# Kernel tuning notes

Hardware: AMD Instinct MI355X
Metric: run time of the kernel (lower is better)

The kernel has to match this reference:

```python
import jax, jax.numpy as jnp
import numpy as np
from jax import lax

B, S, N, F = 64, 512, 30, 1
H, HD = 2, 8              # n_heads, head_dim (gat_hidden=16)
GH = H * HD               # gat_hidden
P = 64                    # projection_dim
LH = 64                   # lstm_hidden
ALPHA = 0.2


def setup_inputs() -> dict:
    key = jax.random.key(0)
    ks = jax.random.split(key, 16)
    x = jax.random.normal(ks[0], (B, S, N, F), dtype=jnp.float32)
    adj = jax.random.randint(ks[1], (N, N), 0, 2).astype(jnp.float32)
    adj = jnp.maximum(adj, jnp.eye(N, dtype=jnp.float32))  # self-loops, no empty rows
    sc = 0.1
    W_gat = sc * jax.random.normal(ks[2], (H, F, HD), dtype=jnp.float32)
    a_src = sc * jax.random.normal(ks[3], (H, HD), dtype=jnp.float32)
    a_dst = sc * jax.random.normal(ks[4], (H, HD), dtype=jnp.float32)
    W_proj = sc * jax.random.normal(ks[5], (N * GH, P), dtype=jnp.float32)
    b_proj = jnp.zeros((P,), dtype=jnp.float32)
    W_ih0 = sc * jax.random.normal(ks[6], (4 * LH, P), dtype=jnp.float32)
    W_hh0 = sc * jax.random.normal(ks[7], (4 * LH, LH), dtype=jnp.float32)
    b_ih0 = jnp.zeros((4 * LH,), dtype=jnp.float32)
    b_hh0 = jnp.zeros((4 * LH,), dtype=jnp.float32)
    W_ih1 = sc * jax.random.normal(ks[8], (4 * LH, LH), dtype=jnp.float32)
    W_hh1 = sc * jax.random.normal(ks[9], (4 * LH, LH), dtype=jnp.float32)
    b_ih1 = jnp.zeros((4 * LH,), dtype=jnp.float32)
    b_hh1 = jnp.zeros((4 * LH,), dtype=jnp.float32)
    W_out = sc * jax.random.normal(ks[10], (LH, N * F), dtype=jnp.float32)
    b_out = jnp.zeros((N * F,), dtype=jnp.float32)
    return dict(x=x, adj=adj, W_gat=W_gat, a_src=a_src, a_dst=a_dst,
                W_proj=W_proj, b_proj=b_proj,
                W_ih0=W_ih0, W_hh0=W_hh0, b_ih0=b_ih0, b_hh0=b_hh0,
                W_ih1=W_ih1, W_hh1=W_hh1, b_ih1=b_ih1, b_hh1=b_hh1,
                W_out=W_out, b_out=b_out)


def _gat(x_flat, adj, W_gat, a_src, a_dst):
    # x_flat: (BS, N, F)
    h = jnp.einsum('bnf,hfd->bhnd', x_flat, W_gat)          # (BS, H, N, HD)
    e_src = jnp.einsum('bhnd,hd->bhn', h, a_src)
    e_dst = jnp.einsum('bhnd,hd->bhn', h, a_dst)
    e = e_src[..., :, None] + e_dst[..., None, :]           # (BS, H, N, N)
    e = jnp.where(e >= 0, e, ALPHA * e)                     # leaky_relu
    e = jnp.where(adj == 0, -jnp.inf, e)
    attn = jax.nn.softmax(e, axis=-1)
    attn = jnp.nan_to_num(attn, nan=0.0)
    out = jnp.einsum('bhij,bhjd->bhid', attn, h)            # (BS, H, N, HD)
    out = jnp.swapaxes(out, 1, 2).reshape(out.shape[0], N, GH)  # head-concat
    out = jnp.where(out > 0, out, jnp.expm1(out))           # elu
    attn_avg = attn.mean(axis=1)                            # (BS, N, N)
    return out, attn_avg


def _lstm_layer(xs, W_ih, W_hh, b_ih, b_hh):
    # xs: (B, S, D) -> (B, S, LH); torch gate order i,f,g,o
    b = xs.shape[0]
    h0 = jnp.zeros((b, LH), xs.dtype)
    c0 = jnp.zeros((b, LH), xs.dtype)

    def step(carry, x_t):
        h, c = carry
        gates = x_t @ W_ih.T + b_ih + h @ W_hh.T + b_hh
        i, f, g, o = jnp.split(gates, 4, axis=-1)
        i, f, o = jax.nn.sigmoid(i), jax.nn.sigmoid(f), jax.nn.sigmoid(o)
        g = jnp.tanh(g)
        c = f * c + i * g
        h = o * jnp.tanh(c)
        return (h, c), h

    (_, _), hs = lax.scan(step, (h0, c0), jnp.swapaxes(xs, 0, 1))
    return jnp.swapaxes(hs, 0, 1)


def reference(x, adj, W_gat, a_src, a_dst, W_proj, b_proj,
              W_ih0, W_hh0, b_ih0, b_hh0, W_ih1, W_hh1, b_ih1, b_hh1,
              W_out, b_out):
    b, s, n, f = x.shape
    x_flat = x.reshape(b * s, n, f)
    gat_out, attn = _gat(x_flat, adj, W_gat, a_src, a_dst)   # (BS,N,GH),(BS,N,N)
    gat_seq = gat_out.reshape(b, s, n * GH)
    gat_seq = jax.nn.relu(gat_seq @ W_proj + b_proj)         # (B,S,P)
    h1 = _lstm_layer(gat_seq, W_ih0, W_hh0, b_ih0, b_hh0)
    h2 = _lstm_layer(h1, W_ih1, W_hh1, b_ih1, b_hh1)
    recon = h2 @ W_out + b_out                               # (B,S,N*F)
    attn_last = attn.reshape(b, s, n, n)[:, -1]              # (B,N,N)
    return recon, attn_last
```

## Files before the change

kernel.cpp:

```cpp
#include <hip/hip_runtime.h>
#include <math.h>

#define BS_TOT 32768
#define NN 30
#define HHD 8
#define GHH 16
#define LHH 64
#define SSS 512
#define BBB 64
#define RECON_SIZE (BBB*SSS*NN)

__device__ __forceinline__ float fsigmoid(float x) {
    return 1.f / (1.f + __expf(-x));
}
__device__ __forceinline__ float ftanh(float x) {
    float ax = fabsf(x);
    float e = __expf(-2.f * ax);
    float r = (1.f - e) / (1.f + e);
    return copysignf(r, x);
}

#define NB 16
__global__ __launch_bounds__(256) void gat_proj_kernel(
    const float* __restrict__ x, const float* __restrict__ adj,
    const float* __restrict__ W_gat, const float* __restrict__ a_src,
    const float* __restrict__ a_dst, const float* __restrict__ W_proj,
    const float* __restrict__ b_proj, float* __restrict__ gat_seq,
    float* __restrict__ attn_out)
{
    __shared__ __align__(16) float gat[NB][480];
    __shared__ __align__(16) float wchunk[96*64];
    __shared__ float x_s[NB][32];
    __shared__ unsigned adjbits[32];

    const int t = threadIdx.x;
    const int bs_base = blockIdx.x * NB;

    for (int rep = 0; rep < 2; ++rep) {
        int idx = rep*256 + t;
        int bl = idx >> 5, j = idx & 31;
        if (j < NN) x_s[bl][j] = x[(bs_base + bl)*NN + j];
    }
    if (t < NN) {
        unsigned bits = 0;
        for (int j = 0; j < NN; ++j)
            if (adj[t*NN + j] != 0.0f) bits |= (1u << j);
        adjbits[t] = bits;
    }
    __syncthreads();

    const int wave = t >> 6, lane = t & 63;
    const int h = lane >> 5, i = lane & 31;
    const bool act = (i < NN);

    float wg[HHD];
    float s_h = 0.f, t_h = 0.f;
    #pragma unroll
    for (int d = 0; d < HHD; ++d) {
        float w = W_gat[h*HHD + d];
        wg[d] = w;
        s_h += w * a_src[h*HHD + d];
        t_h += w * a_dst[h*HHD + d];
    }

    for (int r = 0; r < 4; ++r) {
        const int bl = wave*4 + r;
        const int bs = bs_base + bl;
        const unsigned bits = act ? adjbits[i & 31] : 0u;
        const float xi = act ? x_s[bl][i] : 0.f;
        const float esrc = xi * s_h;

        float m = -1e30f;
        for (int j = 0; j < NN; ++j) {
            if (bits & (1u << j)) {
                float e = esrc + x_s[bl][j] * t_h;
                e = (e >= 0.f) ? e : 0.2f * e;
                m = fmaxf(m, e);
            }
        }
        float Z = 0.f, Sx = 0.f;
        for (int j = 0; j < NN; ++j) {
            if (bits & (1u << j)) {
                float e = esrc + x_s[bl][j] * t_h;
                e = (e >= 0.f) ? e : 0.2f * e;
                float p = expf(e - m);
                Z += p;
                Sx += p * x_s[bl][j];
            }
        }
        const float wsum = Sx / Z;

        if (act) {
            float tmp[8];
            #pragma unroll
            for (int d = 0; d < 8; ++d) {
                float v = wsum * wg[d];
                tmp[d] = (v > 0.f) ? v : expm1f(v);
            }
            float4 v0 = make_float4(tmp[0], tmp[1], tmp[2], tmp[3]);
            float4 v1 = make_float4(tmp[4], tmp[5], tmp[6], tmp[7]);
            *(float4*)&gat[bl][i*GHH + h*HHD]     = v0;
            *(float4*)&gat[bl][i*GHH + h*HHD + 4] = v1;
        }

        if ((bs & (SSS-1)) == (SSS-1)) {
            const int b = bs >> 9;
            for (int j = 0; j < NN; ++j) {
                float a = 0.f;
                if (bits & (1u << j)) {
                    float e = esrc + x_s[bl][j] * t_h;
                    e = (e >= 0.f) ? e : 0.2f * e;
                    a = expf(e - m) / Z;
                }
                float ao = __shfl_xor(a, 32, 64);
                if (act && h == 0)
                    attn_out[b*(NN*NN) + i*NN + j] = 0.5f * (a + ao);
            }
        }
    }
    __syncthreads();

    const int p = t & 63, grp = t >> 6;
    float acc0 = 0.f, acc1 = 0.f, acc2 = 0.f, acc3 = 0.f;
    for (int c = 0; c < 5; ++c) {
        #pragma unroll
        for (int rep = 0; rep < 24; ++rep)
            wchunk[rep*256 + t] = W_proj[c*6144 + rep*256 + t];
        __syncthreads();
        for (int kk = 0; kk < 96; kk += 4) {
            float4 g0 = *(const float4*)&gat[grp*4 + 0][c*96 + kk];
            float4 g1 = *(const float4*)&gat[grp*4 + 1][c*96 + kk];
            float4 g2 = *(const float4*)&gat[grp*4 + 2][c*96 + kk];
            float4 g3 = *(const float4*)&gat[grp*4 + 3][c*96 + kk];
            float w0 = wchunk[(kk+0)*64 + p];
            float w1 = wchunk[(kk+1)*64 + p];
            float w2 = wchunk[(kk+2)*64 + p];
            float w3 = wchunk[(kk+3)*64 + p];
            acc0 += g0.x*w0 + g0.y*w1 + g0.z*w2 + g0.w*w3;
            acc1 += g1.x*w0 + g1.y*w1 + g1.z*w2 + g1.w*w3;
            acc2 += g2.x*w0 + g2.y*w1 + g2.z*w2 + g2.w*w3;
            acc3 += g3.x*w0 + g3.y*w1 + g3.z*w2 + g3.w*w3;
        }
        __syncthreads();
    }
    const float bp = b_proj[p];
    gat_seq[(bs_base + grp*4 + 0)*64 + p] = fmaxf(acc0 + bp, 0.f);
    gat_seq[(bs_base + grp*4 + 1)*64 + p] = fmaxf(acc1 + bp, 0.f);
    gat_seq[(bs_base + grp*4 + 2)*64 + p] = fmaxf(acc2 + bp, 0.f);
    gat_seq[(bs_base + grp*4 + 3)*64 + p] = fmaxf(acc3 + bp, 0.f);
}

__global__ __launch_bounds__(512, 2) void lstm_fused_kernel(
    const float* __restrict__ xin,
    const float* __restrict__ W_ih0, const float* __restrict__ W_hh0,
    const float* __restrict__ b_ih0, const float* __restrict__ b_hh0,
    const float* __restrict__ W_ih1, const float* __restrict__ W_hh1,
    const float* __restrict__ b_ih1, const float* __restrict__ b_hh1,
    float* __restrict__ h2_out)
{
    __shared__ __align__(16) float xh[2][128];
    __shared__ float gates[512];

    const int t = threadIdx.x;
    const int b = blockIdx.x;
    const int layer = t >> 8;
    const int g = t & 255;

    const float* __restrict__ Wih = layer ? W_ih1 : W_ih0;
    const float* __restrict__ Whh = layer ? W_hh1 : W_hh0;
    const float bsum = layer ? (b_ih1[g] + b_hh1[g]) : (b_ih0[g] + b_hh0[g]);

    const float* wihp = Wih + g*64;
    const float* whhp = Whh + g*64;

#define LOADW(i) \
    const float4 wi##i = *(const float4*)(wihp + 4*(i)); \
    const float4 wh##i = *(const float4*)(whhp + 4*(i));
    LOADW(0)  LOADW(1)  LOADW(2)  LOADW(3)
    LOADW(4)  LOADW(5)  LOADW(6)  LOADW(7)
    LOADW(8)  LOADW(9)  LOADW(10) LOADW(11)
    LOADW(12) LOADW(13) LOADW(14) LOADW(15)
#undef LOADW

    if (t < 128) xh[1][t] = 0.f;
    else if (t < 192) xh[0][64 + (t - 128)] = 0.f;

    const float* __restrict__ xrow = xin + (size_t)b * SSS * 64;
    float* __restrict__ hrow = h2_out + (size_t)b * SSS * 64;

    const int sect = g >> 6;
    float c = 0.f;
    float xreg = (t < 64) ? xrow[t] : 0.f;

    const float* xb = &xh[layer][0];

    for (int tt = 0; tt <= SSS; ++tt) {
        if (t < 64 && tt < SSS) xh[0][t] = xreg;
        __syncthreads();
        if (t < 64 && tt + 1 < SSS) xreg = xrow[(tt+1)*64 + t];

        float s0=0.f,s1=0.f,s2=0.f,s3=0.f,s4=0.f,s5=0.f,s6=0.f,s7=0.f;
#define STEPX(i, S) { float4 v = *(const float4*)(xb + 4*(i)); \
        S = fmaf(v.x, wi##i.x, S); S = fmaf(v.y, wi##i.y, S); \
        S = fmaf(v.z, wi##i.z, S); S = fmaf(v.w, wi##i.w, S); }
#define STEPH(i, S) { float4 v = *(const float4*)(xb + 64 + 4*(i)); \
        S = fmaf(v.x, wh##i.x, S); S = fmaf(v.y, wh##i.y, S); \
        S = fmaf(v.z, wh##i.z, S); S = fmaf(v.w, wh##i.w, S); }
        STEPX(0,s0)  STEPX(1,s1)  STEPX(2,s2)  STEPX(3,s3)
        STEPX(4,s4)  STEPX(5,s5)  STEPX(6,s6)  STEPX(7,s7)
        STEPX(8,s0)  STEPX(9,s1)  STEPX(10,s2) STEPX(11,s3)
        STEPX(12,s4) STEPX(13,s5) STEPX(14,s6) STEPX(15,s7)
        STEPH(0,s0)  STEPH(1,s1)  STEPH(2,s2)  STEPH(3,s3)
        STEPH(4,s4)  STEPH(5,s5)  STEPH(6,s6)  STEPH(7,s7)
        STEPH(8,s0)  STEPH(9,s1)  STEPH(10,s2) STEPH(11,s3)
        STEPH(12,s4) STEPH(13,s5) STEPH(14,s6) STEPH(15,s7)
#undef STEPX
#undef STEPH
        float acc = bsum + (((s0+s1)+(s2+s3)) + ((s4+s5)+(s6+s7)));
        float a = (sect == 2) ? ftanh(acc) : fsigmoid(acc);
        gates[t] = a;
        __syncthreads();

        if (t < 64) {
            if (tt < SSS) {
                float ig = gates[t], fg = gates[64+t], gg = gates[128+t], og = gates[192+t];
                c = fg*c + ig*gg;
                float hv = og * ftanh(c);
                xh[0][64+t] = hv;
                xh[1][t]    = hv;
            }
        } else if (t >= 256 && t < 320) {
            if (tt >= 1) {
                int u = t - 256;
                float ig = gates[256+u], fg = gates[320+u], gg = gates[384+u], og = gates[448+u];
                c = fg*c + ig*gg;
                float hv = og * ftanh(c);
                xh[1][64+u] = hv;
                hrow[(size_t)(tt-1)*64 + u] = hv;
            }
        }
    }
}

__global__ __launch_bounds__(256) void recon_kernel(
    const float* __restrict__ h2, const float* __restrict__ W_out,
    const float* __restrict__ b_out, float* __restrict__ out)
{
    __shared__ __align__(16) float hl[8*64];
    const int t = threadIdx.x;
    const int bs_base = blockIdx.x * 8;

    hl[t]       = h2[(size_t)bs_base*64 + t];
    hl[256 + t] = h2[(size_t)bs_base*64 + 256 + t];
    __syncthreads();

    if (t < 240) {
        const int bl = t / 30;
        const int n  = t - bl*30;
        float acc = b_out[n];
        #pragma unroll
        for (int k = 0; k < 64; ++k)
            acc += hl[bl*64 + k] * W_out[k*NN + n];
        out[(size_t)(bs_base + bl)*NN + n] = acc;
    }
}

extern "C" void kernel_launch(void* const* d_in, const int* in_sizes, int n_in,
                              void* d_out, int out_size, void* d_ws, size_t ws_size,
                              hipStream_t stream)
{
    const float* x      = (const float*)d_in[0];
    const float* adj    = (const float*)d_in[1];
    const float* W_gat  = (const float*)d_in[2];
    const float* a_src  = (const float*)d_in[3];
    const float* a_dst  = (const float*)d_in[4];
    const float* W_proj = (const float*)d_in[5];
    const float* b_proj = (const float*)d_in[6];
    const float* W_ih0  = (const float*)d_in[7];
    const float* W_hh0  = (const float*)d_in[8];
    const float* b_ih0  = (const float*)d_in[9];
    const float* b_hh0  = (const float*)d_in[10];
    const float* W_ih1  = (const float*)d_in[11];
    const float* W_hh1  = (const float*)d_in[12];
    const float* b_ih1  = (const float*)d_in[13];
    const float* b_hh1  = (const float*)d_in[14];
    const float* W_out  = (const float*)d_in[15];
    const float* b_out  = (const float*)d_in[16];

    float* out = (float*)d_out;
    float* gat_seq = (float*)d_ws;
    float* h2 = gat_seq + (size_t)BS_TOT*64;

    hipLaunchKernelGGL(gat_proj_kernel, dim3(BS_TOT/NB), dim3(256), 0, stream,
                       x, adj, W_gat, a_src, a_dst, W_proj, b_proj,
                       gat_seq, out + RECON_SIZE);
    hipLaunchKernelGGL(lstm_fused_kernel, dim3(BBB), dim3(512), 0, stream,
                       gat_seq, W_ih0, W_hh0, b_ih0, b_hh0,
                       W_ih1, W_hh1, b_ih1, b_hh1, h2);
    hipLaunchKernelGGL(recon_kernel, dim3(BS_TOT/8), dim3(256), 0, stream,
                       h2, W_out, b_out, out);
}
```

Measured before the change: 735.9 us.

## Halve LSTM block to 4 waves, two gate rows per thread with pinned weights

The fused two-layer LSTM kernel drops from 512 to 256 threads. Each thread now holds two gate rows (256 weight floats, pinned in VGPRs with asm) and computes both dot products from one shared-memory read of the input. Wave 0 ends up holding the i and f gates of layer 0 in registers and wave 2 those of layer 1, so only the g and o gates go through shared memory as float2. This cuts the number of waves synchronised per timestep and the shared-memory traffic on the serial recurrence, at the cost of heavy register pressure and twice the serial FMA work per thread.

```diff
diff --git a/kernel.cpp b/kernel.cpp
--- a/kernel.cpp
+++ b/kernel.cpp
@@ -150,7 +150,7 @@
     gat_seq[(bs_base + grp*4 + 3)*64 + p] = fmaxf(acc3 + bp, 0.f);
 }
 
-__global__ __launch_bounds__(512, 2) void lstm_fused_kernel(
+__global__ __launch_bounds__(256, 1) void lstm_fused4_kernel(
     const float* __restrict__ xin,
     const float* __restrict__ W_ih0, const float* __restrict__ W_hh0,
     const float* __restrict__ b_ih0, const float* __restrict__ b_hh0,
@@ -159,84 +159,99 @@
     float* __restrict__ h2_out)
 {
     __shared__ __align__(16) float xh[2][128];
-    __shared__ float gates[512];
+    __shared__ __align__(8)  float2 go[2][64];
 
     const int t = threadIdx.x;
     const int b = blockIdx.x;
-    const int layer = t >> 8;
-    const int g = t & 255;
-
-    const float* __restrict__ Wih = layer ? W_ih1 : W_ih0;
-    const float* __restrict__ Whh = layer ? W_hh1 : W_hh0;
-    const float bsum = layer ? (b_ih1[g] + b_hh1[g]) : (b_ih0[g] + b_hh0[g]);
-
-    const float* wihp = Wih + g*64;
-    const float* whhp = Whh + g*64;
-
-#define LOADW(i) \
-    const float4 wi##i = *(const float4*)(wihp + 4*(i)); \
-    const float4 wh##i = *(const float4*)(whhp + 4*(i));
-    LOADW(0)  LOADW(1)  LOADW(2)  LOADW(3)
-    LOADW(4)  LOADW(5)  LOADW(6)  LOADW(7)
-    LOADW(8)  LOADW(9)  LOADW(10) LOADW(11)
-    LOADW(12) LOADW(13) LOADW(14) LOADW(15)
-#undef LOADW
-
-    if (t < 128) xh[1][t] = 0.f;
-    else if (t < 192) xh[0][64 + (t - 128)] = 0.f;
+    const int wave = t >> 6, lane = t & 63;
+    const int l = wave >> 1, p = wave & 1;
+    const int rowA = (2*p)*64 + lane;
+    const int rowB = (2*p+1)*64 + lane;
+
+    const float* __restrict__ Wih = l ? W_ih1 : W_ih0;
+    const float* __restrict__ Whh = l ? W_hh1 : W_hh0;
+    const float* __restrict__ bih = l ? b_ih1 : b_ih0;
+    const float* __restrict__ bhh = l ? b_hh1 : b_hh0;
+
+    const float biasA = bih[rowA] + bhh[rowA];
+    const float biasB = bih[rowB] + bhh[rowB];
+
+    const float* wApi = Wih + rowA*64;
+    const float* wBpi = Wih + rowB*64;
+    const float* wAph = Whh + rowA*64;
+    const float* wBph = Whh + rowB*64;
+
+#define LW(i) \
+    float4 wA##i = *(const float4*)(((i) < 16) ? (wApi + 4*(i)) : (wAph + 4*(i) - 64)); \
+    float4 wB##i = *(const float4*)(((i) < 16) ? (wBpi + 4*(i)) : (wBph + 4*(i) - 64));
+    LW(0)  LW(1)  LW(2)  LW(3)  LW(4)  LW(5)  LW(6)  LW(7)
+    LW(8)  LW(9)  LW(10) LW(11) LW(12) LW(13) LW(14) LW(15)
+    LW(16) LW(17) LW(18) LW(19) LW(20) LW(21) LW(22) LW(23)
+    LW(24) LW(25) LW(26) LW(27) LW(28) LW(29) LW(30) LW(31)
+#undef LW
+
+#define PIN(i) asm volatile("" \
+    : "+v"(wA##i.x), "+v"(wA##i.y), "+v"(wA##i.z), "+v"(wA##i.w), \
+      "+v"(wB##i.x), "+v"(wB##i.y), "+v"(wB##i.z), "+v"(wB##i.w));
+    PIN(0)  PIN(1)  PIN(2)  PIN(3)  PIN(4)  PIN(5)  PIN(6)  PIN(7)
+    PIN(8)  PIN(9)  PIN(10) PIN(11) PIN(12) PIN(13) PIN(14) PIN(15)
+    PIN(16) PIN(17) PIN(18) PIN(19) PIN(20) PIN(21) PIN(22) PIN(23)
+    PIN(24) PIN(25) PIN(26) PIN(27) PIN(28) PIN(29) PIN(30) PIN(31)
+#undef PIN
+
+    ((float*)xh)[t] = 0.f;
 
     const float* __restrict__ xrow = xin + (size_t)b * SSS * 64;
     float* __restrict__ hrow = h2_out + (size_t)b * SSS * 64;
 
-    const int sect = g >> 6;
     float c = 0.f;
-    float xreg = (t < 64) ? xrow[t] : 0.f;
-
-    const float* xb = &xh[layer][0];
+    float xreg = (wave == 0) ? xrow[lane] : 0.f;
+    const float* base = xh[l];
 
     for (int tt = 0; tt <= SSS; ++tt) {
-        if (t < 64 && tt < SSS) xh[0][t] = xreg;
+        if (wave == 0 && tt < SSS) xh[0][lane] = xreg;
         __syncthreads();
-        if (t < 64 && tt + 1 < SSS) xreg = xrow[(tt+1)*64 + t];
-
-        float s0=0.f,s1=0.f,s2=0.f,s3=0.f,s4=0.f,s5=0.f,s6=0.f,s7=0.f;
-#define STEPX(i, S) { float4 v = *(const float4*)(xb + 4*(i)); \
-        S = fmaf(v.x, wi##i.x, S); S = fmaf(v.y, wi##i.y, S); \
-        S = fmaf(v.z, wi##i.z, S); S = fmaf(v.w, wi##i.w, S); }
-#define STEPH(i, S) { float4 v = *(const float4*)(xb + 64 + 4*(i)); \
-        S = fmaf(v.x, wh##i.x, S); S = fmaf(v.y, wh##i.y, S); \
-        S = fmaf(v.z, wh##i.z, S); S = fmaf(v.w, wh##i.w, S); }
-        STEPX(0,s0)  STEPX(1,s1)  STEPX(2,s2)  STEPX(3,s3)
-        STEPX(4,s4)  STEPX(5,s5)  STEPX(6,s6)  STEPX(7,s7)
-        STEPX(8,s0)  STEPX(9,s1)  STEPX(10,s2) STEPX(11,s3)
-        STEPX(12,s4) STEPX(13,s5) STEPX(14,s6) STEPX(15,s7)
-        STEPH(0,s0)  STEPH(1,s1)  STEPH(2,s2)  STEPH(3,s3)
-        STEPH(4,s4)  STEPH(5,s5)  STEPH(6,s6)  STEPH(7,s7)
-        STEPH(8,s0)  STEPH(9,s1)  STEPH(10,s2) STEPH(11,s3)
-        STEPH(12,s4) STEPH(13,s5) STEPH(14,s6) STEPH(15,s7)
-#undef STEPX
-#undef STEPH
-        float acc = bsum + (((s0+s1)+(s2+s3)) + ((s4+s5)+(s6+s7)));
-        float a = (sect == 2) ? ftanh(acc) : fsigmoid(acc);
-        gates[t] = a;
+        if (wave == 0 && tt + 1 < SSS) xreg = xrow[(tt+1)*64 + lane];
+
+        float aA0=0.f,aA1=0.f,aA2=0.f,aA3=0.f;
+        float aB0=0.f,aB1=0.f,aB2=0.f,aB3=0.f;
+#define STEP(i, SA, SB) { float4 v = *(const float4*)(base + 4*(i)); \
+        SA = fmaf(v.x, wA##i.x, SA); SA = fmaf(v.y, wA##i.y, SA); \
+        SA = fmaf(v.z, wA##i.z, SA); SA = fmaf(v.w, wA##i.w, SA); \
+        SB = fmaf(v.x, wB##i.x, SB); SB = fmaf(v.y, wB##i.y, SB); \
+        SB = fmaf(v.z, wB##i.z, SB); SB = fmaf(v.w, wB##i.w, SB); }
+        STEP(0,aA0,aB0)  STEP(1,aA1,aB1)  STEP(2,aA2,aB2)  STEP(3,aA3,aB3)
+        STEP(4,aA0,aB0)  STEP(5,aA1,aB1)  STEP(6,aA2,aB2)  STEP(7,aA3,aB3)
+        STEP(8,aA0,aB0)  STEP(9,aA1,aB1)  STEP(10,aA2,aB2) STEP(11,aA3,aB3)
+        STEP(12,aA0,aB0) STEP(13,aA1,aB1) STEP(14,aA2,aB2) STEP(15,aA3,aB3)
+        STEP(16,aA0,aB0) STEP(17,aA1,aB1) STEP(18,aA2,aB2) STEP(19,aA3,aB3)
+        STEP(20,aA0,aB0) STEP(21,aA1,aB1) STEP(22,aA2,aB2) STEP(23,aA3,aB3)
+        STEP(24,aA0,aB0) STEP(25,aA1,aB1) STEP(26,aA2,aB2) STEP(27,aA3,aB3)
+        STEP(28,aA0,aB0) STEP(29,aA1,aB1) STEP(30,aA2,aB2) STEP(31,aA3,aB3)
+#undef STEP
+        const float gA = biasA + ((aA0+aA1)+(aA2+aA3));
+        const float gB = biasB + ((aB0+aB1)+(aB2+aB3));
+        float actA, actB;
+        if (p == 0) { actA = fsigmoid(gA); actB = fsigmoid(gB); }
+        else        { actA = ftanh(gA);    actB = fsigmoid(gB); }
+        if (p == 1) go[l][lane] = make_float2(actA, actB);
         __syncthreads();
 
-        if (t < 64) {
+        if (wave == 0) {
             if (tt < SSS) {
-                float ig = gates[t], fg = gates[64+t], gg = gates[128+t], og = gates[192+t];
-                c = fg*c + ig*gg;
-                float hv = og * ftanh(c);
-                xh[0][64+t] = hv;
-                xh[1][t]    = hv;
-            }
-        } else if (t >= 256 && t < 320) {
+                float2 g2 = go[0][lane];
+                c = actB * c + actA * g2.x;
+                float u = g2.y * ftanh(c);
+                xh[0][64 + lane] = u;
+                xh[1][lane]      = u;
+            }
+        } else if (wave == 2) {
             if (tt >= 1) {
-                int u = t - 256;
-                float ig = gates[256+u], fg = gates[320+u], gg = gates[384+u], og = gates[448+u];
-                c = fg*c + ig*gg;
-                float hv = og * ftanh(c);
-                xh[1][64+u] = hv;
-                hrow[(size_t)(tt-1)*64 + u] = hv;
+                float2 g2 = go[1][lane];
+                c = actB * c + actA * g2.x;
+                float v = g2.y * ftanh(c);
+                xh[1][64 + lane] = v;
+                hrow[(size_t)(tt-1)*64 + lane] = v;
             }
         }
     }
@@ -294,7 +309,7 @@
     hipLaunchKernelGGL(gat_proj_kernel, dim3(BS_TOT/NB), dim3(256), 0, stream,
                        x, adj, W_gat, a_src, a_dst, W_proj, b_proj,
                        gat_seq, out + RECON_SIZE);
-    hipLaunchKernelGGL(lstm_fused_kernel, dim3(BBB), dim3(512), 0, stream,
+    hipLaunchKernelGGL(lstm_fused4_kernel, dim3(BBB), dim3(256), 0, stream,
                        gat_seq, W_ih0, W_hh0, b_ih0, b_hh0,
                        W_ih1, W_hh1, b_ih1, b_hh1, h2);
     hipLaunchKernelGGL(recon_kernel, dim3(BS_TOT/8), dim3(256), 0, stream,
```

Result: slower. 881.4 us (+19.8%).
